# Kernel tuning notes

Hardware: AMD Instinct MI355X
Metric: run time of the kernel (lower is better)

Reference implementation:

```python
import jax, jax.numpy as jnp
import numpy as np

B, L, E, H = 2, 2048, 1024, 16
HD = E // H


def _rel_shift(x):
    # x: [b, h, q, k] -> Transformer-XL relative shift via pad+reshape trick
    b, h, q, k = x.shape
    xp = jnp.pad(x, ((0, 0), (0, 0), (0, 0), (1, 0)))  # pad left of last dim
    xp = xp.reshape(b, h, k + 1, q)
    return xp[:, :, 1:, :].reshape(b, h, q, k)


def setup_inputs() -> dict:
    key = jax.random.key(0)
    ks = jax.random.split(key, 16)
    s = 0.02
    return {
        "query": jax.random.normal(ks[0], (B, L, E), jnp.float32),
        "key": jax.random.normal(ks[1], (B, L, E), jnp.float32),
        "value": jax.random.normal(ks[2], (B, L, E), jnp.float32),
        "pos_embedding": jax.random.normal(ks[3], (B, L, E), jnp.float32),
        "Wq": jax.random.normal(ks[4], (E, E), jnp.float32) * s,
        "bq": jnp.zeros((E,), jnp.float32),
        "Wk": jax.random.normal(ks[5], (E, E), jnp.float32) * s,
        "bk": jnp.zeros((E,), jnp.float32),
        "Wv": jax.random.normal(ks[6], (E, E), jnp.float32) * s,
        "bv": jnp.zeros((E,), jnp.float32),
        "Wp": jax.random.normal(ks[7], (E, E), jnp.float32) * s,  # Pos linear, no bias
        "Wo": jax.random.normal(ks[8], (E, E), jnp.float32) * s,
        "bo": jnp.zeros((E,), jnp.float32),
        "U": jax.random.normal(ks[9], (H, HD), jnp.float32) * s,
        "V": jax.random.normal(ks[10], (H, HD), jnp.float32) * s,
    }


def reference(query, key, value, pos_embedding, Wq, bq, Wk, bk, Wv, bv, Wp, Wo, bo, U, V):
    b, qlen, e = query.shape
    h, hd = U.shape
    scale = jnp.sqrt(jnp.asarray(e, query.dtype))
    # torch Linear: y = x @ W.T + b
    q = (query @ Wq.T + bq).reshape(b, qlen, h, hd)
    k = (key @ Wk.T + bk).reshape(b, key.shape[1], h, hd)
    v = (value @ Wv.T + bv).reshape(b, value.shape[1], h, hd)
    r = (pos_embedding @ Wp.T).reshape(b, -1, h, hd)
    content_score = jnp.einsum("bqhd,bkhd->bhqk", q + U, k)
    position_score = jnp.einsum("bqhd,bkhd->bhqk", q + V, r)
    position_score = _rel_shift(position_score)
    attention_score = (content_score + position_score) / scale
    # NOTE: the original module applies NO softmax; faithful reproduction.
    # einsum 'bhqk,bvhd->bqhd' sums over both k (scores) and v (values).
    alpha = jnp.einsum("bhqk,bvhd->bqhd", attention_score, v).reshape(b, qlen, e)
    return alpha @ Wo.T + bo
```

## Files before the change

### kernel.cpp

```cpp
#include <hip/hip_runtime.h>

#define BB 2
#define LL 2048
#define EE 1024
#define HH 16
#define HDD 64

typedef __bf16 bf16x8 __attribute__((ext_vector_type(8)));
typedef float f32x4 __attribute__((ext_vector_type(4)));

__device__ __forceinline__ unsigned short f2bf(float f) {
  unsigned int x = __float_as_uint(f);
  return (unsigned short)((x + 0x7FFFu + ((x >> 16) & 1u)) >> 16);
}

__device__ __forceinline__ float bf2f(unsigned short u) {
  return __uint_as_float((unsigned int)u << 16);
}

__device__ __forceinline__ void load_lds16(const void* g, void* l) {
  __builtin_amdgcn_global_load_lds(
      (const __attribute__((address_space(1))) void*)g,
      (__attribute__((address_space(3))) void*)l, 16, 0, 0);
}

#define SUMKV_BLOCKS 256
#define CAST_BLOCKS 1280
#define CAST_STRIDE (CAST_BLOCKS * 256)
__global__ __launch_bounds__(256) void prelude_kernel(
    const float* __restrict__ q, const float* __restrict__ pe,
    const float* __restrict__ wq, const float* __restrict__ wp,
    unsigned short* __restrict__ q16, unsigned short* __restrict__ pe16,
    unsigned short* __restrict__ wq16, unsigned short* __restrict__ wp16,
    const float* __restrict__ key, const float* __restrict__ value,
    float* __restrict__ keysum, float* __restrict__ valsum) {
  if (blockIdx.x < SUMKV_BLOCKS) {
    int blk2 = blockIdx.x;
    int b = blk2 >> 7, ch = blk2 & 127;
    int tid = threadIdx.x;
    const float4* k4 = (const float4*)(key   + ((size_t)b * LL + ch * 16) * EE);
    const float4* v4 = (const float4*)(value + ((size_t)b * LL + ch * 16) * EE);
    float4 ak = make_float4(0.f, 0.f, 0.f, 0.f);
    float4 av = make_float4(0.f, 0.f, 0.f, 0.f);
#pragma unroll 8
    for (int i = 0; i < 16; i++) {
      float4 kk = k4[i * 256 + tid];
      float4 vv = v4[i * 256 + tid];
      ak.x += kk.x; ak.y += kk.y; ak.z += kk.z; ak.w += kk.w;
      av.x += vv.x; av.y += vv.y; av.z += vv.z; av.w += vv.w;
    }
    int e = tid * 4;
    atomicAdd(&keysum[b * EE + e + 0], ak.x);
    atomicAdd(&keysum[b * EE + e + 1], ak.y);
    atomicAdd(&keysum[b * EE + e + 2], ak.z);
    atomicAdd(&keysum[b * EE + e + 3], ak.w);
    atomicAdd(&valsum[b * EE + e + 0], av.x);
    atomicAdd(&valsum[b * EE + e + 1], av.y);
    atomicAdd(&valsum[b * EE + e + 2], av.z);
    atomicAdd(&valsum[b * EE + e + 3], av.w);
  } else {
    const int NQ4 = BB * LL * EE / 4;
    const int NW4 = EE * EE / 4;
    int t = (blockIdx.x - SUMKV_BLOCKS) * 256 + threadIdx.x;
    float4 v[8]; unsigned short* dst[8]; int off[8];
#pragma unroll
    for (int k = 0; k < 8; k++) {
      int i = t + k * CAST_STRIDE;
      const float* src;
      if (i < NQ4)                { src = q;  dst[k] = q16;  off[k] = i; }
      else if (i < 2 * NQ4)       { src = pe; dst[k] = pe16; off[k] = i - NQ4; }
      else if (i < 2 * NQ4 + NW4) { src = wq; dst[k] = wq16; off[k] = i - 2 * NQ4; }
      else                        { src = wp; dst[k] = wp16; off[k] = i - 2 * NQ4 - NW4; }
      v[k] = ((const float4*)src)[off[k]];
    }
#pragma unroll
    for (int k = 0; k < 8; k++) {
      ushort4 u;
      u.x = f2bf(v[k].x); u.y = f2bf(v[k].y); u.z = f2bf(v[k].z); u.w = f2bf(v[k].w);
      ((ushort4*)dst[k])[off[k]] = u;
    }
  }
}

__global__ __launch_bounds__(256) void proj_kernel(
    const float* __restrict__ keysum, const float* __restrict__ valsum,
    const float* __restrict__ Wk, const float* __restrict__ bk,
    const float* __restrict__ Wv, const float* __restrict__ bv,
    float* __restrict__ Kproj, float* __restrict__ Vproj) {
  int wv = threadIdx.x >> 6, lane = threadIdx.x & 63;
  int idx = blockIdx.x * 4 + wv;
  int b = idx >> 10, ep = idx & (EE - 1);
  const float* sum  = blockIdx.z ? valsum : keysum;
  const float* W    = blockIdx.z ? Wv : Wk;
  const float* bias = blockIdx.z ? bv : bk;
  float* outp       = blockIdx.z ? Vproj : Kproj;
  float acc = 0.f;
  for (int k = lane; k < EE; k += 64) acc += sum[b * EE + k] * W[ep * EE + k];
  for (int off = 32; off; off >>= 1) acc += __shfl_down(acc, off, 64);
  if (lane == 0) outp[b * EE + ep] = acc + (float)LL * bias[ep];
}

__global__ __launch_bounds__(256) void gemm_kernel(
    const unsigned short* __restrict__ q16, const unsigned short* __restrict__ wq16,
    const float* __restrict__ bq, unsigned short* __restrict__ qout,
    const unsigned short* __restrict__ pe16, const unsigned short* __restrict__ wp16,
    unsigned short* __restrict__ rout, float* __restrict__ chunks,
    const float* __restrict__ Vproj, const float* __restrict__ Wo,
    float* __restrict__ W2) {
  const int tid = threadIdx.x;
  const int lane = tid & 63;
  const int wv = tid >> 6;

  if (blockIdx.z == 2) {
    int bid = blockIdx.x + 32 * blockIdx.y;
    int wslot = bid * 4 + wv;
    int base = wslot * 32;
    int b = base >> 14;
    int h = (base >> 10) & (HH - 1);
    int e0 = base & (EE - 1);
    float vp = Vproj[b * EE + h * HDD + lane];
    const float* wo = Wo + (size_t)e0 * EE + h * HDD + lane;
    for (int r = 0; r < 32; r++) {
      float acc = vp * wo[(size_t)r * EE];
      for (int off = 32; off; off >>= 1) acc += __shfl_down(acc, off, 64);
      if (lane == 0) W2[((size_t)b * HH + h) * EE + e0 + r] = acc;
    }
    return;
  }

  const int K = EE, N = EE;
  const unsigned short* X; const unsigned short* W; const float* bias;
  unsigned short* Out;
  if (blockIdx.z == 0) { X = q16;  W = wq16; bias = bq;      Out = qout; }
  else                 { X = pe16; W = wp16; bias = nullptr; Out = rout; }

  __shared__ __align__(16) unsigned short As[2][128 * 32];
  __shared__ __align__(16) unsigned short Bs[2][128 * 32];

  const int wr = wv >> 1, wc = wv & 1;
  const int m0 = blockIdx.x * 128;
  const int n0 = blockIdx.y * 128;

  const int srow = wv * 16 + (lane >> 2);
  const int s_src = ((lane & 3) - ((lane >> 3) & 3)) & 3;
  const unsigned short* gA = X + (size_t)(m0 + srow) * K + s_src * 8;
  const unsigned short* gB = W + (size_t)(n0 + srow) * K + s_src * 8;

  f32x4 acc[4][4];
#pragma unroll
  for (int i = 0; i < 4; i++)
#pragma unroll
    for (int j = 0; j < 4; j++) acc[i][j] = (f32x4)0.0f;

  const int arow = wr * 64 + (lane & 15);
  const int brow = wc * 64 + (lane & 15);
  const int koff = (((lane >> 4) + ((lane & 15) >> 1)) & 3) * 8;

#define GSTAGE(BI, KK)                                                   \
  do {                                                                   \
    load_lds16(gA + (KK),                  &As[BI][wv * 512]);           \
    load_lds16(gA + (KK) + (size_t)64 * K, &As[BI][wv * 512 + 2048]);    \
    load_lds16(gB + (KK),                  &Bs[BI][wv * 512]);           \
    load_lds16(gB + (KK) + (size_t)64 * K, &Bs[BI][wv * 512 + 2048]);    \
  } while (0)

  GSTAGE(0, 0);
  __syncthreads();
  int bi = 0;
  for (int t = 0; t < K / 32; ++t) {
    if (t + 1 < K / 32) GSTAGE(bi ^ 1, (t + 1) * 32);
    bf16x8 af[4], bf[4];
#pragma unroll
    for (int i = 0; i < 4; i++)
      af[i] = *(const bf16x8*)&As[bi][(arow + i * 16) * 32 + koff];
#pragma unroll
    for (int j = 0; j < 4; j++)
      bf[j] = *(const bf16x8*)&Bs[bi][(brow + j * 16) * 32 + koff];
#pragma unroll
    for (int i = 0; i < 4; i++)
#pragma unroll
      for (int j = 0; j < 4; j++)
        acc[i][j] = __builtin_amdgcn_mfma_f32_16x16x32_bf16(af[i], bf[j], acc[i][j], 0, 0, 0);
    __syncthreads();
    bi ^= 1;
  }
#undef GSTAGE

  const int rbase = m0 + wr * 64 + (lane >> 4) * 4;
  const int cbase = n0 + wc * 64 + (lane & 15);
#pragma unroll
  for (int i = 0; i < 4; i++) {
#pragma unroll
    for (int j = 0; j < 4; j++) {
      int col = cbase + j * 16;
      float badd = bias ? bias[col] : 0.f;
#pragma unroll
      for (int g = 0; g < 4; g++) {
        int row = rbase + i * 16 + g;
        Out[(size_t)row * N + col] = f2bf(acc[i][j][g] + badd);
      }
    }
  }

  if (blockIdx.z == 1) {
    int b = m0 >> 11;
    int ch0 = ((m0 & (LL - 1)) >> 5) + wr * 2;
#pragma unroll
    for (int cp = 0; cp < 2; cp++) {
#pragma unroll
      for (int j = 0; j < 4; j++) {
        float s = 0.f;
#pragma unroll
        for (int i = cp * 2; i < cp * 2 + 2; i++)
#pragma unroll
          for (int g = 0; g < 4; g++) s += acc[i][j][g];
        s += __shfl_down(s, 32, 64);
        s += __shfl_down(s, 16, 64);
        if (lane < 16) {
          int col = n0 + wc * 64 + j * 16 + lane;
          chunks[((size_t)b * 64 + ch0 + cp) * EE + col] = s;
        }
      }
    }
  }
}

__global__ __launch_bounds__(256) void scan2f_kernel(
    const unsigned short* __restrict__ qbuf, const unsigned short* __restrict__ rbuf,
    const float* __restrict__ chunks, const float* __restrict__ Kproj,
    const float* __restrict__ U, const float* __restrict__ V,
    float* __restrict__ S1, float* __restrict__ Dbuf) {
  int tid = threadIdx.x, lane = tid & 63;
  int hg = blockIdx.x, ch = blockIdx.y, b = blockIdx.z;
  int e = hg * 256 + tid;
  int h = hg * 4 + (tid >> 6);
  float pre = 0.f, tot = 0.f;
  for (int c = 0; c < 64; c++) {
    float cs = chunks[((size_t)b * 64 + c) * EE + e];
    tot += cs;
    if (c < ch) pre += cs;
  }
  float kp = Kproj[b * EE + e], Ue = U[e], Ve = V[e];
  float run = pre;
  size_t hoff = ((size_t)b * HH + h) * LL;
#pragma unroll 4
  for (int i = 0; i < 32; i++) {
    int m = ch * 32 + i;
    int p = LL - 1 - m;
    float qv = bf2f(qbuf[((size_t)b * LL + p) * EE + e]);
    float rv = bf2f(rbuf[((size_t)b * LL + m) * EE + e]);
    float tq = qv + Ve;
    float d = tq * run;
    float s = tq * tot + (qv + Ue) * kp;
#pragma unroll
    for (int off = 32; off; off >>= 1) {
      d += __shfl_down(d, off, 64);
      s += __shfl_down(s, off, 64);
    }
    if (lane == 0) { Dbuf[hoff + m] = d; S1[hoff + p] = s; }
    run += rv;
  }
}

__global__ __launch_bounds__(256) void out_kernel(
    const float* __restrict__ S1, const float* __restrict__ Dbuf,
    const float* __restrict__ W2, const float* __restrict__ bo,
    float* __restrict__ out) {
  int row0 = blockIdx.x * 8;
  int b = row0 >> 11, p0 = row0 & (LL - 1);
  int tid = threadIdx.x;
  __shared__ float sh[8][HH];
  if (tid < 128) {
    int rr = tid >> 4, h = tid & 15;
    int p = p0 + rr;
    size_t hoff = ((size_t)b * HH + h) * LL;
    float s1 = S1[hoff + p];
    float d1 = Dbuf[hoff + (LL - 1 - p)];
    float d2 = (p == LL - 1) ? 0.f : Dbuf[hoff + (LL - 2 - p)];
    sh[rr][h] = (s1 - d1 + d2) * (1.f / 32.f);
  }
  float4 w2r[HH];
#pragma unroll
  for (int h = 0; h < HH; h++)
    w2r[h] = ((const float4*)(W2 + ((size_t)b * HH + h) * EE))[tid];
  float4 bo4 = ((const float4*)bo)[tid];
  __syncthreads();
#pragma unroll
  for (int rr = 0; rr < 8; rr++) {
    float4 acc = bo4;
#pragma unroll
    for (int h = 0; h < HH; h++) {
      float s = sh[rr][h];
      acc.x += s * w2r[h].x; acc.y += s * w2r[h].y;
      acc.z += s * w2r[h].z; acc.w += s * w2r[h].w;
    }
    ((float4*)out)[(size_t)(row0 + rr) * 256 + tid] = acc;
  }
}

extern "C" void kernel_launch(void* const* d_in, const int* in_sizes, int n_in,
                              void* d_out, int out_size, void* d_ws, size_t ws_size,
                              hipStream_t stream) {
  const float* query = (const float*)d_in[0];
  const float* key   = (const float*)d_in[1];
  const float* value = (const float*)d_in[2];
  const float* pos   = (const float*)d_in[3];
  const float* Wq = (const float*)d_in[4];
  const float* bq = (const float*)d_in[5];
  const float* Wk = (const float*)d_in[6];
  const float* bk = (const float*)d_in[7];
  const float* Wv = (const float*)d_in[8];
  const float* bv = (const float*)d_in[9];
  const float* Wp = (const float*)d_in[10];
  const float* Wo = (const float*)d_in[11];
  const float* bo = (const float*)d_in[12];
  const float* U  = (const float*)d_in[13];
  const float* V  = (const float*)d_in[14];
  float* out = (float*)d_out;

  char* ws = (char*)d_ws;
  size_t o = 0;
  auto take = [&](size_t bytes) -> char* {
    char* p = ws + o;
    o += (bytes + 255) & ~(size_t)255;
    return p;
  };
  float* keysum = (float*)take(BB * EE * 4);
  float* valsum = (float*)take(BB * EE * 4);
  float* Kproj  = (float*)take(BB * EE * 4);
  float* Vproj  = (float*)take(BB * EE * 4);
  float* W2     = (float*)take((size_t)BB * HH * EE * 4);
  float* S1     = (float*)take((size_t)BB * HH * LL * 4);
  float* Dbuf   = (float*)take((size_t)BB * HH * LL * 4);
  float* chunks = (float*)take((size_t)BB * 64 * EE * 4);
  unsigned short* qbuf = (unsigned short*)take((size_t)BB * LL * EE * 2);
  unsigned short* rbuf = (unsigned short*)take((size_t)BB * LL * EE * 2);
  unsigned short* q16  = (unsigned short*)take((size_t)BB * LL * EE * 2);
  unsigned short* pe16 = (unsigned short*)take((size_t)BB * LL * EE * 2);
  unsigned short* wq16 = (unsigned short*)take((size_t)EE * EE * 2);
  unsigned short* wp16 = (unsigned short*)take((size_t)EE * EE * 2);

  hipMemsetAsync(keysum, 0, (size_t)2 * BB * EE * 4, stream);

  prelude_kernel<<<SUMKV_BLOCKS + CAST_BLOCKS, 256, 0, stream>>>(
      query, pos, Wq, Wp, q16, pe16, wq16, wp16, key, value, keysum, valsum);
  proj_kernel<<<dim3(BB * EE / 4, 1, 2), 256, 0, stream>>>(
      keysum, valsum, Wk, bk, Wv, bv, Kproj, Vproj);
  gemm_kernel<<<dim3(BB * LL / 128, EE / 128, 3), 256, 0, stream>>>(
      q16, wq16, bq, qbuf, pe16, wp16, rbuf, chunks, Vproj, Wo, W2);
  scan2f_kernel<<<dim3(4, 64, BB), 256, 0, stream>>>(qbuf, rbuf, chunks, Kproj, U, V, S1, Dbuf);
  out_kernel<<<dim3(BB * LL / 8), 256, 0, stream>>>(S1, Dbuf, W2, bo, out);
}
```

Measured before the change: 226.5 us.

## Triple-buffer GEMM, replace atomics with partial-sum reduce, halve scan chunk size

Several changes at once. The GEMM main loop moves from double to triple buffering, using explicit vmcnt waits and a raw barrier so global-to-LDS loads run two stages ahead; launch bounds also request 3 blocks per SM. The key/value column sums now write per-chunk partials that a new small reduce kernel adds up, replacing float atomics and the memset. The chunk size for the scan is halved from 32 to 16 rows, doubling the scan grid and the chunk-sum buffer. This costs extra LDS, an additional kernel launch and more partial-sum traffic.

```diff
diff --git a/kernel.cpp b/kernel.cpp
--- a/kernel.cpp
+++ b/kernel.cpp
@@ -33,7 +33,7 @@
     unsigned short* __restrict__ q16, unsigned short* __restrict__ pe16,
     unsigned short* __restrict__ wq16, unsigned short* __restrict__ wp16,
     const float* __restrict__ key, const float* __restrict__ value,
-    float* __restrict__ keysum, float* __restrict__ valsum) {
+    float* __restrict__ kpart, float* __restrict__ vpart) {
   if (blockIdx.x < SUMKV_BLOCKS) {
     int blk2 = blockIdx.x;
     int b = blk2 >> 7, ch = blk2 & 127;
@@ -49,15 +49,8 @@
       ak.x += kk.x; ak.y += kk.y; ak.z += kk.z; ak.w += kk.w;
       av.x += vv.x; av.y += vv.y; av.z += vv.z; av.w += vv.w;
     }
-    int e = tid * 4;
-    atomicAdd(&keysum[b * EE + e + 0], ak.x);
-    atomicAdd(&keysum[b * EE + e + 1], ak.y);
-    atomicAdd(&keysum[b * EE + e + 2], ak.z);
-    atomicAdd(&keysum[b * EE + e + 3], ak.w);
-    atomicAdd(&valsum[b * EE + e + 0], av.x);
-    atomicAdd(&valsum[b * EE + e + 1], av.y);
-    atomicAdd(&valsum[b * EE + e + 2], av.z);
-    atomicAdd(&valsum[b * EE + e + 3], av.w);
+    ((float4*)(kpart + ((size_t)b * 128 + ch) * EE))[tid] = ak;
+    ((float4*)(vpart + ((size_t)b * 128 + ch) * EE))[tid] = av;
   } else {
     const int NQ4 = BB * LL * EE / 4;
     const int NW4 = EE * EE / 4;
@@ -80,6 +73,19 @@
       ((ushort4*)dst[k])[off[k]] = u;
     }
   }
+}
+
+__global__ __launch_bounds__(256) void reduce_kernel(
+    const float* __restrict__ kpart, const float* __restrict__ vpart,
+    float* __restrict__ keysum, float* __restrict__ valsum) {
+  int idx = blockIdx.x * 256 + threadIdx.x;
+  const float* src = (idx & 2048) ? vpart : kpart;
+  float* dst = (idx & 2048) ? valsum : keysum;
+  int be = idx & 2047;
+  int b = be >> 10, e = be & (EE - 1);
+  float s = 0.f;
+  for (int c = 0; c < 128; c++) s += src[((size_t)b * 128 + c) * EE + e];
+  dst[be] = s;
 }
 
 __global__ __launch_bounds__(256) void proj_kernel(
@@ -100,7 +106,7 @@
   if (lane == 0) outp[b * EE + ep] = acc + (float)LL * bias[ep];
 }
 
-__global__ __launch_bounds__(256) void gemm_kernel(
+__global__ __launch_bounds__(256, 3) void gemm_kernel(
     const unsigned short* __restrict__ q16, const unsigned short* __restrict__ wq16,
     const float* __restrict__ bq, unsigned short* __restrict__ qout,
     const unsigned short* __restrict__ pe16, const unsigned short* __restrict__ wp16,
@@ -134,8 +140,8 @@
   if (blockIdx.z == 0) { X = q16;  W = wq16; bias = bq;      Out = qout; }
   else                 { X = pe16; W = wp16; bias = nullptr; Out = rout; }
 
-  __shared__ __align__(16) unsigned short As[2][128 * 32];
-  __shared__ __align__(16) unsigned short Bs[2][128 * 32];
+  __shared__ __align__(16) unsigned short As[3][128 * 32];
+  __shared__ __align__(16) unsigned short Bs[3][128 * 32];
 
   const int wr = wv >> 1, wc = wv & 1;
   const int m0 = blockIdx.x * 128;
@@ -156,35 +162,40 @@
   const int brow = wc * 64 + (lane & 15);
   const int koff = (((lane >> 4) + ((lane & 15) >> 1)) & 3) * 8;
 
-#define GSTAGE(BI, KK)                                                   \
-  do {                                                                   \
-    load_lds16(gA + (KK),                  &As[BI][wv * 512]);           \
-    load_lds16(gA + (KK) + (size_t)64 * K, &As[BI][wv * 512 + 2048]);    \
-    load_lds16(gB + (KK),                  &Bs[BI][wv * 512]);           \
-    load_lds16(gB + (KK) + (size_t)64 * K, &Bs[BI][wv * 512 + 2048]);    \
+#define GSTAGE(BI, KK)                                                    \
+  do {                                                                    \
+    load_lds16(gA + (KK),                  &As[BI][wv * 512]);            \
+    load_lds16(gA + (KK) + (size_t)64 * K, &As[BI][wv * 512 + 2048]);     \
+    load_lds16(gB + (KK),                  &Bs[BI][wv * 512]);            \
+    load_lds16(gB + (KK) + (size_t)64 * K, &Bs[BI][wv * 512 + 2048]);     \
   } while (0)
+#define COMPUTE(BI)                                                       \
+  do {                                                                    \
+    bf16x8 af[4], bf[4];                                                  \
+    _Pragma("unroll") for (int i = 0; i < 4; i++)                         \
+      af[i] = *(const bf16x8*)&As[BI][(arow + i * 16) * 32 + koff];       \
+    _Pragma("unroll") for (int j = 0; j < 4; j++)                         \
+      bf[j] = *(const bf16x8*)&Bs[BI][(brow + j * 16) * 32 + koff];       \
+    _Pragma("unroll") for (int i = 0; i < 4; i++)                         \
+    _Pragma("unroll") for (int j = 0; j < 4; j++)                         \
+      acc[i][j] = __builtin_amdgcn_mfma_f32_16x16x32_bf16(af[i], bf[j],   \
+                                                          acc[i][j], 0, 0, 0); \
+  } while (0)
 
   GSTAGE(0, 0);
-  __syncthreads();
-  int bi = 0;
-  for (int t = 0; t < K / 32; ++t) {
-    if (t + 1 < K / 32) GSTAGE(bi ^ 1, (t + 1) * 32);
-    bf16x8 af[4], bf[4];
-#pragma unroll
-    for (int i = 0; i < 4; i++)
-      af[i] = *(const bf16x8*)&As[bi][(arow + i * 16) * 32 + koff];
-#pragma unroll
-    for (int j = 0; j < 4; j++)
-      bf[j] = *(const bf16x8*)&Bs[bi][(brow + j * 16) * 32 + koff];
-#pragma unroll
-    for (int i = 0; i < 4; i++)
-#pragma unroll
-      for (int j = 0; j < 4; j++)
-        acc[i][j] = __builtin_amdgcn_mfma_f32_16x16x32_bf16(af[i], bf[j], acc[i][j], 0, 0, 0);
-    __syncthreads();
-    bi ^= 1;
+  GSTAGE(1, 32);
+  int c0 = 0, c1 = 1, c2 = 2;
+  for (int t = 0; t < 32; ++t) {
+    if (t < 31) asm volatile("s_waitcnt vmcnt(4)" ::: "memory");
+    else        asm volatile("s_waitcnt vmcnt(0)" ::: "memory");
+    __builtin_amdgcn_s_barrier();
+    __builtin_amdgcn_sched_barrier(0);
+    if (t + 2 < 32) GSTAGE(c2, (t + 2) * 32);
+    COMPUTE(c0);
+    int tmp = c0; c0 = c1; c1 = c2; c2 = tmp;
   }
 #undef GSTAGE
+#undef COMPUTE
 
   const int rbase = m0 + wr * 64 + (lane >> 4) * 4;
   const int cbase = n0 + wc * 64 + (lane & 15);
@@ -204,21 +215,17 @@
 
   if (blockIdx.z == 1) {
     int b = m0 >> 11;
-    int ch0 = ((m0 & (LL - 1)) >> 5) + wr * 2;
-#pragma unroll
-    for (int cp = 0; cp < 2; cp++) {
+    int ch0 = ((m0 + wr * 64) & (LL - 1)) >> 4;
+#pragma unroll
+    for (int i = 0; i < 4; i++) {
 #pragma unroll
       for (int j = 0; j < 4; j++) {
-        float s = 0.f;
-#pragma unroll
-        for (int i = cp * 2; i < cp * 2 + 2; i++)
-#pragma unroll
-          for (int g = 0; g < 4; g++) s += acc[i][j][g];
+        float s = acc[i][j][0] + acc[i][j][1] + acc[i][j][2] + acc[i][j][3];
         s += __shfl_down(s, 32, 64);
         s += __shfl_down(s, 16, 64);
         if (lane < 16) {
           int col = n0 + wc * 64 + j * 16 + lane;
-          chunks[((size_t)b * 64 + ch0 + cp) * EE + col] = s;
+          chunks[((size_t)b * 128 + ch0 + i) * EE + col] = s;
         }
       }
     }
@@ -235,8 +242,8 @@
   int e = hg * 256 + tid;
   int h = hg * 4 + (tid >> 6);
   float pre = 0.f, tot = 0.f;
-  for (int c = 0; c < 64; c++) {
-    float cs = chunks[((size_t)b * 64 + c) * EE + e];
+  for (int c = 0; c < 128; c++) {
+    float cs = chunks[((size_t)b * 128 + c) * EE + e];
     tot += cs;
     if (c < ch) pre += cs;
   }
@@ -244,8 +251,8 @@
   float run = pre;
   size_t hoff = ((size_t)b * HH + h) * LL;
 #pragma unroll 4
-  for (int i = 0; i < 32; i++) {
-    int m = ch * 32 + i;
+  for (int i = 0; i < 16; i++) {
+    int m = ch * 16 + i;
     int p = LL - 1 - m;
     float qv = bf2f(qbuf[((size_t)b * LL + p) * EE + e]);
     float rv = bf2f(rbuf[((size_t)b * LL + m) * EE + e]);
@@ -332,7 +339,9 @@
   float* W2     = (float*)take((size_t)BB * HH * EE * 4);
   float* S1     = (float*)take((size_t)BB * HH * LL * 4);
   float* Dbuf   = (float*)take((size_t)BB * HH * LL * 4);
-  float* chunks = (float*)take((size_t)BB * 64 * EE * 4);
+  float* chunks = (float*)take((size_t)BB * 128 * EE * 4);
+  float* kpart  = (float*)take((size_t)BB * 128 * EE * 4);
+  float* vpart  = (float*)take((size_t)BB * 128 * EE * 4);
   unsigned short* qbuf = (unsigned short*)take((size_t)BB * LL * EE * 2);
   unsigned short* rbuf = (unsigned short*)take((size_t)BB * LL * EE * 2);
   unsigned short* q16  = (unsigned short*)take((size_t)BB * LL * EE * 2);
@@ -340,14 +349,14 @@
   unsigned short* wq16 = (unsigned short*)take((size_t)EE * EE * 2);
   unsigned short* wp16 = (unsigned short*)take((size_t)EE * EE * 2);
 
-  hipMemsetAsync(keysum, 0, (size_t)2 * BB * EE * 4, stream);
-
   prelude_kernel<<<SUMKV_BLOCKS + CAST_BLOCKS, 256, 0, stream>>>(
-      query, pos, Wq, Wp, q16, pe16, wq16, wp16, key, value, keysum, valsum);
+      query, pos, Wq, Wp, q16, pe16, wq16, wp16, key, value, kpart, vpart);
+  reduce_kernel<<<dim3(16), 256, 0, stream>>>(kpart, vpart, keysum, valsum);
   proj_kernel<<<dim3(BB * EE / 4, 1, 2), 256, 0, stream>>>(
       keysum, valsum, Wk, bk, Wv, bv, Kproj, Vproj);
   gemm_kernel<<<dim3(BB * LL / 128, EE / 128, 3), 256, 0, stream>>>(
       q16, wq16, bq, qbuf, pe16, wp16, rbuf, chunks, Vproj, Wo, W2);
-  scan2f_kernel<<<dim3(4, 64, BB), 256, 0, stream>>>(qbuf, rbuf, chunks, Kproj, U, V, S1, Dbuf);
+  scan2f_kernel<<<dim3(4, 128, BB), 256, 0, stream>>>(
+      qbuf, rbuf, chunks, Kproj, U, V, S1, Dbuf);
   out_kernel<<<dim3(BB * LL / 8), 256, 0, stream>>>(S1, Dbuf, W2, bo, out);
 }
```

Result: faster. 210.4 us (-7.1%).
